# Kernel tuning notes

Measured on AMD Instinct MI355X. Metric: run time of the kernel, lower is better.

The kernel has to match this reference:

```python
import jax, jax.numpy as jnp
import numpy as np

V, E, H, L = 50257, 512, 512, 2
PAD_ID = 50256


def setup_inputs() -> dict:
    key = jax.random.key(0)
    ks = jax.random.split(key, 24)
    B, TD, TE = 16, 64, 256
    s = 0.02
    emb = jax.random.normal(ks[0], (V, E), jnp.float32) * s
    emb = emb.at[PAD_ID].set(0.0)  # padding_idx row is zero
    inp = {
        "dec_input_ids": jax.random.randint(ks[1], (B, TD), 0, V, jnp.int32),
        "initial_hidden": jax.random.normal(ks[2], (L, B, H), jnp.float32),
        "initial_cell": jax.random.normal(ks[3], (L, B, H), jnp.float32),
        "encoder_outputs": jax.random.normal(ks[4], (B, TE, H), jnp.float32),
        "src_mask": jax.random.randint(ks[5], (B, TE), 0, 2, jnp.int32),
        "emb": emb,
        "W1_w": jax.random.normal(ks[6], (H, H), jnp.float32) * s,
        "W1_b": jnp.zeros((H,), jnp.float32),
        "W2_w": jax.random.normal(ks[7], (H, H), jnp.float32) * s,
        "W2_b": jnp.zeros((H,), jnp.float32),
        "v_w": jax.random.normal(ks[8], (H,), jnp.float32) * s,
        "v_b": jnp.zeros((), jnp.float32),
        "W_ih0": jax.random.normal(ks[9], (4 * H, E + H), jnp.float32) * s,
        "W_hh0": jax.random.normal(ks[10], (4 * H, H), jnp.float32) * s,
        "b_ih0": jnp.zeros((4 * H,), jnp.float32),
        "b_hh0": jnp.zeros((4 * H,), jnp.float32),
        "W_ih1": jax.random.normal(ks[11], (4 * H, H), jnp.float32) * s,
        "W_hh1": jax.random.normal(ks[12], (4 * H, H), jnp.float32) * s,
        "b_ih1": jnp.zeros((4 * H,), jnp.float32),
        "b_hh1": jnp.zeros((4 * H,), jnp.float32),
        "fc_w": jax.random.normal(ks[13], (V, H), jnp.float32) * s,
        "fc_b": jnp.zeros((V,), jnp.float32),
    }
    return inp


def _lstm_cell(x, h, c, Wi, Wh, bi, bh):
    g = x @ Wi.T + bi + h @ Wh.T + bh  # (B, 4H)
    i, f, gg, o = jnp.split(g, 4, axis=-1)  # PyTorch gate order i,f,g,o
    i, f, o = jax.nn.sigmoid(i), jax.nn.sigmoid(f), jax.nn.sigmoid(o)
    gg = jnp.tanh(gg)
    cn = f * c + i * gg
    hn = o * jnp.tanh(cn)
    return hn, cn


def reference(dec_input_ids, initial_hidden, initial_cell, encoder_outputs, src_mask,
              emb, W1_w, W1_b, W2_w, W2_b, v_w, v_b,
              W_ih0, W_hh0, b_ih0, b_hh0, W_ih1, W_hh1, b_ih1, b_hh1,
              fc_w, fc_b):
    embedded = emb[dec_input_ids]                      # (B, T_dec, E)
    enc_proj = encoder_outputs @ W1_w.T + W1_b         # W1(encoder_outputs), (B, T_enc, H)
    pad = src_mask == 0                                # (B, T_enc)
    layers = ((W_ih0, W_hh0, b_ih0, b_hh0), (W_ih1, W_hh1, b_ih1, b_hh1))

    def step(carry, emb_t):
        h, c = carry                                   # each (L, B, H)
        q = h[-1] @ W2_w.T + W2_b                      # (B, H)
        score = jnp.tanh(enc_proj + q[:, None, :]) @ v_w + v_b  # (B, T_enc)
        score = jnp.where(pad, -1e9, score)
        attn = jax.nn.softmax(score, axis=-1)
        context = jnp.einsum('bt,bth->bh', attn, encoder_outputs)
        x = jnp.concatenate([emb_t, context], axis=-1)  # (B, E+H)
        hs, cs = [], []
        for l, (Wi, Wh, bi, bh) in enumerate(layers):
            hn, cn = _lstm_cell(x, h[l], c[l], Wi, Wh, bi, bh)
            hs.append(hn); cs.append(cn)
            x = hn
        logits_t = x @ fc_w.T + fc_b                    # (B, V)
        return (jnp.stack(hs), jnp.stack(cs)), logits_t

    _, logits = jax.lax.scan(step, (initial_hidden, initial_cell),
                             jnp.swapaxes(embedded, 0, 1))  # (T_dec, B, V)
    return jnp.swapaxes(logits, 0, 1)                       # (B, T_dec, V)
```

## Files before the change

### kernel.cpp

```cpp
#include <hip/hip_runtime.h>

#define DI __device__ __forceinline__

typedef __attribute__((ext_vector_type(2))) float f32x2;
typedef __attribute__((ext_vector_type(4))) float f32x4;
typedef __attribute__((ext_vector_type(8))) short bf16x8;
typedef __attribute__((ext_vector_type(8))) unsigned short u16x8;

constexpr int Vv = 50257, NPAD = 50304, Ee = 512, Hh = 512, Bb = 16, TDn = 64, TEn = 256;
constexpr int NBLK = 64;

constexpr size_t OFF_ENCP = 0;
constexpr size_t OFF_ENCT = OFF_ENCP + (size_t)Bb*TEn*Hh*4;
constexpr size_t OFF_G0E  = OFF_ENCT + (size_t)Bb*Hh*TEn*4;
constexpr size_t OFF_FCWB = OFF_G0E  + (size_t)TDn*Bb*4*Hh*4;
constexpr size_t OFF_H1B  = OFF_FCWB + (size_t)NPAD*Hh*2;
constexpr size_t OFF_Q    = OFF_H1B  + (size_t)TDn*Bb*Hh*2;
constexpr size_t OFF_SC   = OFF_Q    + (size_t)Bb*Hh*4;
constexpr size_t OFF_CTX  = OFF_SC   + (size_t)Bb*TEn*4;
constexpr size_t OFF_H0   = OFF_CTX  + (size_t)Bb*Hh*4;
constexpr size_t OFF_H1   = OFF_H0   + (size_t)2*Bb*Hh*4;
constexpr size_t OFF_SYNC = OFF_H1   + (size_t)2*Bb*Hh*4;

DI float dot4(f32x4 a, f32x4 b) { return a[0]*b[0] + a[1]*b[1] + a[2]*b[2] + a[3]*b[3]; }
DI float wsum(float v) { for (int m = 32; m; m >>= 1) v += __shfl_xor(v, m, 64); return v; }
DI float wmax(float v) { for (int m = 32; m; m >>= 1) v = fmaxf(v, __shfl_xor(v, m, 64)); return v; }
DI void wsum4(float& a, float& b, float& c, float& d) {
    #pragma unroll
    for (int m = 32; m; m >>= 1) {
        a += __shfl_xor(a, m, 64);
        b += __shfl_xor(b, m, 64);
        c += __shfl_xor(c, m, 64);
        d += __shfl_xor(d, m, 64);
    }
}
DI float tanhfast(float x) { float e = __expf(2.f * x); return 1.f - 2.f / (e + 1.f); }
DI float sigm(float x) { return 1.f / (1.f + __expf(-x)); }

DI int swz(int a) { return a ^ (((a >> 5) & 7) << 2); }

DI float gload1(const float* p) {
    return __hip_atomic_load(p, __ATOMIC_RELAXED, __HIP_MEMORY_SCOPE_AGENT);
}
DI void gstore1(float* p, float v) {
    __hip_atomic_store(p, v, __ATOMIC_RELAXED, __HIP_MEMORY_SCOPE_AGENT);
}
DI f32x2 gload2(const float* p) {
    unsigned long long u = __hip_atomic_load((const unsigned long long*)p,
                                             __ATOMIC_RELAXED, __HIP_MEMORY_SCOPE_AGENT);
    return __builtin_bit_cast(f32x2, u);
}
DI void gstore2(float* p, f32x2 v) {
    __hip_atomic_store((unsigned long long*)p, __builtin_bit_cast(unsigned long long, v),
                       __ATOMIC_RELAXED, __HIP_MEMORY_SCOPE_AGENT);
}
DI f32x4 gload4(const float* p) {
    f32x2 a = gload2(p), b = gload2(p + 2);
    f32x4 r; r[0] = a[0]; r[1] = a[1]; r[2] = b[0]; r[3] = b[1];
    return r;
}
DI void gstoreu16(unsigned short* p, unsigned short v) {
    __hip_atomic_store(p, v, __ATOMIC_RELAXED, __HIP_MEMORY_SCOPE_AGENT);
}

DI unsigned short f2bf(float f) {
    unsigned u = __builtin_bit_cast(unsigned, f);
    unsigned r = (u + 0x7FFFu + ((u >> 16) & 1u)) >> 16;
    return (unsigned short)r;
}
DI u16x8 cvt8(f32x4 a, f32x4 b) {
    u16x8 r;
    r[0]=f2bf(a[0]); r[1]=f2bf(a[1]); r[2]=f2bf(a[2]); r[3]=f2bf(a[3]);
    r[4]=f2bf(b[0]); r[5]=f2bf(b[1]); r[6]=f2bf(b[2]); r[7]=f2bf(b[3]);
    return r;
}

DI void gsync(unsigned* cnt, unsigned* gen, unsigned k) {
    __syncthreads();
    if (threadIdx.x == 0) {
        asm volatile("s_waitcnt vmcnt(0)" ::: "memory");
        unsigned old = __hip_atomic_fetch_add(cnt, 1u, __ATOMIC_RELAXED, __HIP_MEMORY_SCOPE_AGENT);
        if (old == k * (unsigned)NBLK - 1u) {
            __hip_atomic_store(gen, k, __ATOMIC_RELAXED, __HIP_MEMORY_SCOPE_AGENT);
        } else {
            int spins = 0;
            while (true) {
                unsigned g = __hip_atomic_load(gen, __ATOMIC_RELAXED, __HIP_MEMORY_SCOPE_AGENT);
                if (g >= k) break;
                __builtin_amdgcn_s_sleep(1);
                if ((++spins & 1023) == 0) {
                    g = __hip_atomic_load(gen, __ATOMIC_ACQUIRE, __HIP_MEMORY_SCOPE_AGENT);
                    if (g >= k) break;
                }
            }
        }
        asm volatile("" ::: "memory");
    }
    __syncthreads();
}

__global__ void prep_fcw_kernel(const float* __restrict__ src, unsigned short* __restrict__ dst) {
    size_t i = ((size_t)blockIdx.x * 256 + threadIdx.x) << 3;
    int n = (int)(i >> 9);
    u16x8 v = {0,0,0,0,0,0,0,0};
    if (n < Vv) {
        const float* p = src + i;
        v = cvt8(*(const f32x4*)p, *(const f32x4*)(p + 4));
    }
    *(u16x8*)(dst + i) = v;
}

__global__ void transpose_kernel(const float* __restrict__ enc, float* __restrict__ encT) {
    __shared__ float tile[32][33];
    const int b = blockIdx.z, e0 = blockIdx.x << 5, h0 = blockIdx.y << 5;
    const int tx = threadIdx.x, ty = threadIdx.y;
    #pragma unroll
    for (int i = 0; i < 4; ++i)
        tile[ty + i*8][tx] = enc[((size_t)(b*TEn + e0 + ty + i*8))*Hh + h0 + tx];
    __syncthreads();
    #pragma unroll
    for (int i = 0; i < 4; ++i)
        encT[((size_t)(b*Hh + h0 + ty + i*8))*TEn + e0 + tx] = tile[tx][ty + i*8];
}

template<int SRCBF, int GATHER, int OUTM>
__global__ __launch_bounds__(256, 2) void gemm_bt(
    const void* __restrict__ Av, const void* __restrict__ Bv,
    const float* __restrict__ bias, const float* __restrict__ bias2,
    float* __restrict__ Cout, int M, int N, int K, int ldb,
    const int* __restrict__ ids, int NV)
{
    __shared__ unsigned short As[128*32], Bs[128*32];
    const int tid = threadIdx.x;
    const int bn = blockIdx.x, bm = blockIdx.y;
    const int w = tid >> 6, l = tid & 63;
    const int wm = w >> 1, wn = w & 1;
    const int lr = l & 15, ls = l >> 4;
    f32x4 acc[4][4] = {};

    const int r0 = tid >> 2, c0 = (tid & 3) << 3;

    for (int kb = 0; kb < K; kb += 32) {
        #pragma unroll
        for (int half = 0; half < 2; ++half) {
            const int rr = r0 + half*64;
            {
                const int gm = bm*128 + rr;
                size_t arow = GATHER ? (size_t)ids[((gm & 15) << 6) + (gm >> 4)] : (size_t)gm;
                u16x8 v;
                if (SRCBF) {
                    v = *(const u16x8*)((const unsigned short*)Av + arow*(size_t)K + kb + c0);
                } else {
                    const float* ap = (const float*)Av + arow*(size_t)K + kb + c0;
                    v = cvt8(*(const f32x4*)ap, *(const f32x4*)(ap + 4));
                }
                *(u16x8*)&As[rr*32 + c0] = v;
            }
            {
                const size_t brow = (size_t)(bn*128 + rr);
                u16x8 v;
                if (SRCBF) {
                    v = *(const u16x8*)((const unsigned short*)Bv + brow*(size_t)ldb + kb + c0);
                } else {
                    const float* bp = (const float*)Bv + brow*(size_t)ldb + kb + c0;
                    v = cvt8(*(const f32x4*)bp, *(const f32x4*)(bp + 4));
                }
                *(u16x8*)&Bs[rr*32 + c0] = v;
            }
        }
        __syncthreads();
        bf16x8 af[4], bfv[4];
        #pragma unroll
        for (int mt = 0; mt < 4; ++mt) af[mt]  = *(const bf16x8*)&As[(wm*64 + mt*16 + lr)*32 + ls*8];
        #pragma unroll
        for (int nt = 0; nt < 4; ++nt) bfv[nt] = *(const bf16x8*)&Bs[(wn*64 + nt*16 + lr)*32 + ls*8];
        #pragma unroll
        for (int mt = 0; mt < 4; ++mt)
            #pragma unroll
            for (int nt = 0; nt < 4; ++nt)
                acc[mt][nt] = __builtin_amdgcn_mfma_f32_16x16x32_bf16(af[mt], bfv[nt], acc[mt][nt], 0, 0, 0);
        __syncthreads();
    }

    #pragma unroll
    for (int mt = 0; mt < 4; ++mt) {
        #pragma unroll
        for (int nt = 0; nt < 4; ++nt) {
            const int n = bn*128 + wn*64 + nt*16 + lr;
            const int mbase = bm*128 + wm*64 + mt*16 + ls*4;
            f32x4 a = acc[mt][nt];
            #pragma unroll
            for (int r = 0; r < 4; ++r) {
                const int m = mbase + r;
                if (OUTM == 0) {
                    float v = a[r] + bias[n] + (bias2 ? bias2[n] : 0.f);
                    Cout[(size_t)m*N + n] = v;
                } else {
                    if (n < NV) {
                        float v = a[r] + bias[n];
                        Cout[(size_t)(((m & 15) << 6) + (m >> 4))*NV + n] = v;
                    }
                }
            }
        }
    }
}

__global__ __launch_bounds__(512, 1) void recur_kernel(
    const float* __restrict__ ih, const float* __restrict__ ic,
    const float* __restrict__ W2w, const float* __restrict__ W2b,
    const float* __restrict__ vw, const float* __restrict__ vb,
    const int* __restrict__ smask,
    const float* __restrict__ Wi0, const float* __restrict__ Wh0,
    const float* __restrict__ Wi1, const float* __restrict__ Wh1,
    const float* __restrict__ bi1, const float* __restrict__ bh1,
    char* __restrict__ ws)
{
    float* encP = (float*)(ws + OFF_ENCP);
    float* encT = (float*)(ws + OFF_ENCT);
    float* g0e  = (float*)(ws + OFF_G0E);
    unsigned short* h1bf = (unsigned short*)(ws + OFF_H1B);
    float* qb  = (float*)(ws + OFF_Q);
    float* sc  = (float*)(ws + OFF_SC);
    float* ctx = (float*)(ws + OFF_CTX);
    float* h0b = (float*)(ws + OFF_H0);
    float* h1v = (float*)(ws + OFF_H1);
    unsigned* cnt = (unsigned*)(ws + OFF_SYNC);
    unsigned* gen = cnt + 64;

    __shared__ float lds[2 * Bb * Hh];

    const int tid = threadIdx.x, bid = blockIdx.x;
    const int wid = tid >> 6, l = tid & 63;
    const int j  = (bid << 3) + wid;
    const int k0 = l << 3;

    f32x4 wi0a[4], wi0b[4], wh0a[4], wh0b[4];
    f32x4 wi1a[4], wi1b[4], wh1a[4], wh1b[4];
    float bb1[4];
    #pragma unroll
    for (int g = 0; g < 4; ++g) {
        const float* p0 = Wi0 + (size_t)(g*Hh + j)*(Ee + Hh) + Ee + k0;
        wi0a[g] = *(const f32x4*)p0; wi0b[g] = *(const f32x4*)(p0 + 4);
        const float* p1 = Wh0 + (size_t)(g*Hh + j)*Hh + k0;
        wh0a[g] = *(const f32x4*)p1; wh0b[g] = *(const f32x4*)(p1 + 4);
        const float* p2 = Wi1 + (size_t)(g*Hh + j)*Hh + k0;
        wi1a[g] = *(const f32x4*)p2; wi1b[g] = *(const f32x4*)(p2 + 4);
        const float* p3 = Wh1 + (size_t)(g*Hh + j)*Hh + k0;
        wh1a[g] = *(const f32x4*)p3; wh1b[g] = *(const f32x4*)(p3 + 4);
        bb1[g] = bi1[g*Hh + j] + bh1[g*Hh + j];
    }
    const float* wr = W2w + (size_t)j*Hh + k0;
    const f32x4 w2a = *(const f32x4*)wr, w2d = *(const f32x4*)(wr + 4);
    const float w2bias = W2b[j];
    const f32x4 va = *(const f32x4*)&vw[k0], vd = *(const f32x4*)&vw[k0 + 4];
    const float vbias = vb[0];

    float c0r = (l < 16) ? ic[l*Hh + j]           : 0.f;
    float c1r = (l < 16) ? ic[Bb*Hh + l*Hh + j]   : 0.f;

    const int sb  = ((bid >> 5) << 3) | (bid & 7);
    const int u   = ((bid >> 3) & 3) * 8 + wid;
    const int se0 = u << 3;
    const int ch0 = u << 4;
    const int msk = (l < 8) ? smask[sb*TEn + se0 + l] : 1;

    for (int i = bid*512 + tid; i < (Bb*Hh) / 2; i += NBLK*512) {
        gstore2(&h0b[i*2], *(const f32x2*)&ih[i*2]);
        gstore2(&h1v[i*2], *(const f32x2*)&ih[Bb*Hh + i*2]);
    }
    unsigned bk = 0;
    gsync(cnt, gen, ++bk);

    for (int t = 0; t < TDn; ++t) {
        const int p = t & 1;
        const float* h1r = h1v + p*(Bb*Hh);
        float*       h1w = h1v + (p^1)*(Bb*Hh);
        const float* h0r = h0b + p*(Bb*Hh);
        float*       h0w = h0b + (p^1)*(Bb*Hh);

        float ge0 = 0.f, ge1 = 0.f, ge2 = 0.f, ge3 = 0.f;
        if (l < 16) {
            const float* gp = g0e + ((size_t)(t*Bb + l))*(4*Hh) + j;
            ge0 = gp[0]; ge1 = gp[Hh]; ge2 = gp[2*Hh]; ge3 = gp[3*Hh];
        }

        {
            for (int i = tid*2; i < Bb*Hh; i += 1024)
                *(f32x2*)&lds[swz(i)] = gload2(&h1r[i]);
            __syncthreads();
            float qv = 0.f;
            #pragma unroll 4
            for (int b = 0; b < Bb; ++b) {
                f32x4 ha = *(const f32x4*)&lds[swz(b*Hh + k0)];
                f32x4 hd = *(const f32x4*)&lds[swz(b*Hh + k0 + 4)];
                float s = dot4(ha, w2a) + dot4(hd, w2d);
                s = wsum(s);
                qv = (l == b) ? s + w2bias : qv;
            }
            if (l < 16) gstore1(&qb[l*Hh + j], qv);
        }
        gsync(cnt, gen, ++bk);

        {
            f32x4 qa = gload4(&qb[sb*Hh + k0]);
            f32x4 qd = gload4(&qb[sb*Hh + k0 + 4]);
            float myS = 0.f;
            #pragma unroll
            for (int i = 0; i < 8; ++i) {
                const int e = se0 + i;
                const float* ep = encP + ((size_t)(sb*TEn + e))*Hh + k0;
                f32x4 ea = *(const f32x4*)ep, ed = *(const f32x4*)(ep + 4);
                float s = 0.f;
                #pragma unroll
                for (int c = 0; c < 4; ++c)
                    s += tanhfast(ea[c] + qa[c]) * va[c] + tanhfast(ed[c] + qd[c]) * vd[c];
                s = wsum(s);
                myS = (l == i) ? s : myS;
            }
            if (l < 8)
                gstore1(&sc[sb*TEn + se0 + l], (msk == 0) ? -1e9f : (myS + vbias));
        }
        gsync(cnt, gen, ++bk);

        {
            f32x4 s4 = gload4(&sc[sb*TEn + (l << 2)]);
            float mx = wmax(fmaxf(fmaxf(s4[0], s4[1]), fmaxf(s4[2], s4[3])));
            f32x4 e4; float sm = 0.f;
            #pragma unroll
            for (int c = 0; c < 4; ++c) { e4[c] = __expf(s4[c] - mx); sm += e4[c]; }
            sm = wsum(sm);
            const float inv = 1.0f / sm;
            float myC = 0.f;
            #pragma unroll 4
            for (int i = 0; i < 16; ++i) {
                const int h = ch0 + i;
                f32x4 en = *(const f32x4*)&encT[((size_t)(sb*Hh + h))*TEn + (l << 2)];
                float s = wsum(dot4(e4, en));
                myC = (l == i) ? s : myC;
            }
            if (l < 16) gstore1(&ctx[sb*Hh + ch0 + l], myC * inv);
        }
        gsync(cnt, gen, ++bk);

        {
            for (int i = tid*2; i < Bb*Hh; i += 1024) {
                *(f32x2*)&lds[swz(i)]          = gload2(&ctx[i]);
                *(f32x2*)&lds[swz(Bb*Hh + i)]  = gload2(&h0r[i]);
            }
            __syncthreads();
            float ls0 = 0.f, ls1 = 0.f, ls2 = 0.f, ls3 = 0.f;
            #pragma unroll 4
            for (int b = 0; b < Bb; ++b) {
                f32x4 xa = *(const f32x4*)&lds[swz(b*Hh + k0)];
                f32x4 xd = *(const f32x4*)&lds[swz(b*Hh + k0 + 4)];
                f32x4 ha = *(const f32x4*)&lds[swz(Bb*Hh + b*Hh + k0)];
                f32x4 hd = *(const f32x4*)&lds[swz(Bb*Hh + b*Hh + k0 + 4)];
                float s0 = dot4(wi0a[0],xa)+dot4(wi0b[0],xd)+dot4(wh0a[0],ha)+dot4(wh0b[0],hd);
                float s1 = dot4(wi0a[1],xa)+dot4(wi0b[1],xd)+dot4(wh0a[1],ha)+dot4(wh0b[1],hd);
                float s2 = dot4(wi0a[2],xa)+dot4(wi0b[2],xd)+dot4(wh0a[2],ha)+dot4(wh0b[2],hd);
                float s3 = dot4(wi0a[3],xa)+dot4(wi0b[3],xd)+dot4(wh0a[3],ha)+dot4(wh0b[3],hd);
                wsum4(s0, s1, s2, s3);
                if (l == b) { ls0 = s0; ls1 = s1; ls2 = s2; ls3 = s3; }
            }
            if (l < 16) {
                float ii = sigm(ls0 + ge0), ff = sigm(ls1 + ge1);
                float gg = tanhfast(ls2 + ge2), oo = sigm(ls3 + ge3);
                float cn = ff*c0r + ii*gg;
                c0r = cn;
                gstore1(&h0w[l*Hh + j], oo * tanhfast(cn));
            }
        }
        gsync(cnt, gen, ++bk);

        {
            for (int i = tid*2; i < Bb*Hh; i += 1024) {
                *(f32x2*)&lds[swz(i)]          = gload2(&h0w[i]);
                *(f32x2*)&lds[swz(Bb*Hh + i)]  = gload2(&h1r[i]);
            }
            __syncthreads();
            float ls0 = 0.f, ls1 = 0.f, ls2 = 0.f, ls3 = 0.f;
            #pragma unroll 4
            for (int b = 0; b < Bb; ++b) {
                f32x4 xa = *(const f32x4*)&lds[swz(b*Hh + k0)];
                f32x4 xd = *(const f32x4*)&lds[swz(b*Hh + k0 + 4)];
                f32x4 ha = *(const f32x4*)&lds[swz(Bb*Hh + b*Hh + k0)];
                f32x4 hd = *(const f32x4*)&lds[swz(Bb*Hh + b*Hh + k0 + 4)];
                float s0 = dot4(wi1a[0],xa)+dot4(wi1b[0],xd)+dot4(wh1a[0],ha)+dot4(wh1b[0],hd);
                float s1 = dot4(wi1a[1],xa)+dot4(wi1b[1],xd)+dot4(wh1a[1],ha)+dot4(wh1b[1],hd);
                float s2 = dot4(wi1a[2],xa)+dot4(wi1b[2],xd)+dot4(wh1a[2],ha)+dot4(wh1b[2],hd);
                float s3 = dot4(wi1a[3],xa)+dot4(wi1b[3],xd)+dot4(wh1a[3],ha)+dot4(wh1b[3],hd);
                wsum4(s0, s1, s2, s3);
                if (l == b) { ls0 = s0; ls1 = s1; ls2 = s2; ls3 = s3; }
            }
            if (l < 16) {
                float ii = sigm(ls0 + bb1[0]), ff = sigm(ls1 + bb1[1]);
                float gg = tanhfast(ls2 + bb1[2]), oo = sigm(ls3 + bb1[3]);
                float cn = ff*c1r + ii*gg;
                c1r = cn;
                float hn = oo * tanhfast(cn);
                gstore1(&h1w[l*Hh + j], hn);
                gstoreu16(&h1bf[((size_t)(t*Bb + l))*Hh + j], f2bf(hn));
            }
        }
        gsync(cnt, gen, ++bk);
    }
}

extern "C" void kernel_launch(void* const* d_in, const int* in_sizes, int n_in,
                              void* d_out, int out_size, void* d_ws, size_t ws_size,
                              hipStream_t stream)
{
    const int*   ids  = (const int*)d_in[0];
    const float* ih   = (const float*)d_in[1];
    const float* ic   = (const float*)d_in[2];
    const float* enc  = (const float*)d_in[3];
    const int*   smask= (const int*)d_in[4];
    const float* emb  = (const float*)d_in[5];
    const float* W1w  = (const float*)d_in[6];
    const float* W1b  = (const float*)d_in[7];
    const float* W2w  = (const float*)d_in[8];
    const float* W2b  = (const float*)d_in[9];
    const float* vw   = (const float*)d_in[10];
    const float* vb   = (const float*)d_in[11];
    const float* Wi0  = (const float*)d_in[12];
    const float* Wh0  = (const float*)d_in[13];
    const float* bi0  = (const float*)d_in[14];
    const float* bh0  = (const float*)d_in[15];
    const float* Wi1  = (const float*)d_in[16];
    const float* Wh1  = (const float*)d_in[17];
    const float* bi1  = (const float*)d_in[18];
    const float* bh1  = (const float*)d_in[19];
    const float* fcw  = (const float*)d_in[20];
    const float* fcb  = (const float*)d_in[21];
    float* out = (float*)d_out;
    char*  ws  = (char*)d_ws;

    hipMemsetAsync(ws + OFF_SYNC, 0, 2048, stream);

    prep_fcw_kernel<<<dim3((unsigned)((size_t)NPAD*Hh/8/256)), dim3(256), 0, stream>>>(
        fcw, (unsigned short*)(ws + OFF_FCWB));

    transpose_kernel<<<dim3(TEn/32, Hh/32, Bb), dim3(32, 8), 0, stream>>>(
        enc, (float*)(ws + OFF_ENCT));

    gemm_bt<0,0,0><<<dim3(Hh/128, (Bb*TEn)/128), dim3(256), 0, stream>>>(
        enc, W1w, W1b, nullptr, (float*)(ws + OFF_ENCP),
        Bb*TEn, Hh, Hh, Hh, nullptr, 0);

    gemm_bt<0,1,0><<<dim3((4*Hh)/128, (TDn*Bb)/128), dim3(256), 0, stream>>>(
        emb, Wi0, bi0, bh0, (float*)(ws + OFF_G0E),
        TDn*Bb, 4*Hh, Ee, Ee + Hh, ids, 0);

    {
        void* args[] = { (void*)&ih, (void*)&ic, (void*)&W2w, (void*)&W2b,
                         (void*)&vw, (void*)&vb, (void*)&smask,
                         (void*)&Wi0, (void*)&Wh0, (void*)&Wi1, (void*)&Wh1,
                         (void*)&bi1, (void*)&bh1, (void*)&ws };
        hipLaunchCooperativeKernel((void*)recur_kernel, dim3(NBLK), dim3(512), args, 0, stream);
    }

    gemm_bt<1,0,1><<<dim3(NPAD/128, (TDn*Bb)/128), dim3(256), 0, stream>>>(
        ws + OFF_H1B, ws + OFF_FCWB, fcb, nullptr, out,
        TDn*Bb, NPAD, Hh, Hh, nullptr, Vv);
}
```

Before: 3.748 ms.

## Replace atomic-counter grid barrier with flag-array barrier and per-batch group barrier

Swaps the fetch-add counter grid barrier for a barrier where each block writes its own byte flag and one wavefront polls eight 64-bit words for the expected pattern. The score-to-softmax step now uses a barrier among only the 4 blocks that share a batch row, instead of a full grid barrier. Work is remapped so each group of 4 blocks handles one batch element. Global-to-LDS staging loads are widened to 4 floats. The aim is to cut barrier latency and contention on a single atomic in a latency-bound recurrent loop. It relies on byte-sized generation counters wrapping correctly and on using two alternating flag buffers.

```diff
diff --git a/kernel.cpp b/kernel.cpp
--- a/kernel.cpp
+++ b/kernel.cpp
@@ -75,26 +75,40 @@
     return r;
 }
 
-DI void gsync(unsigned* cnt, unsigned* gen, unsigned k) {
+DI void gbar(char* sy, int bid, unsigned kg) {
+    __syncthreads();
+    if (threadIdx.x < 64) {
+        unsigned long long* gf = (unsigned long long*)(sy + ((kg & 1) ? 0 : 512));
+        if (threadIdx.x == 0) {
+            asm volatile("s_waitcnt vmcnt(0)" ::: "memory");
+            char* p = (char*)(gf + (size_t)(bid >> 3) * 8) + (bid & 7);
+            __hip_atomic_store(p, (char)(unsigned char)kg, __ATOMIC_RELAXED, __HIP_MEMORY_SCOPE_AGENT);
+        }
+        const unsigned long long pat = 0x0101010101010101ULL * (unsigned char)kg;
+        const int lane = threadIdx.x;
+        for (;;) {
+            bool ok = true;
+            if (lane < 8)
+                ok = (__hip_atomic_load(gf + (size_t)lane * 8, __ATOMIC_RELAXED,
+                                        __HIP_MEMORY_SCOPE_AGENT) == pat);
+            if (__all(ok)) break;
+            __builtin_amdgcn_s_sleep(1);
+        }
+    }
+    __syncthreads();
+}
+
+DI void rbar(char* sy, int g, int u4, unsigned kr) {
     __syncthreads();
     if (threadIdx.x == 0) {
+        unsigned* gr = (unsigned*)(sy + ((kr & 1) ? 1024 : 2048));
         asm volatile("s_waitcnt vmcnt(0)" ::: "memory");
-        unsigned old = __hip_atomic_fetch_add(cnt, 1u, __ATOMIC_RELAXED, __HIP_MEMORY_SCOPE_AGENT);
-        if (old == k * (unsigned)NBLK - 1u) {
-            __hip_atomic_store(gen, k, __ATOMIC_RELAXED, __HIP_MEMORY_SCOPE_AGENT);
-        } else {
-            int spins = 0;
-            while (true) {
-                unsigned g = __hip_atomic_load(gen, __ATOMIC_RELAXED, __HIP_MEMORY_SCOPE_AGENT);
-                if (g >= k) break;
-                __builtin_amdgcn_s_sleep(1);
-                if ((++spins & 1023) == 0) {
-                    g = __hip_atomic_load(gen, __ATOMIC_ACQUIRE, __HIP_MEMORY_SCOPE_AGENT);
-                    if (g >= k) break;
-                }
-            }
-        }
-        asm volatile("" ::: "memory");
+        char* p = (char*)(gr + (size_t)g * 16) + u4;
+        __hip_atomic_store(p, (char)(unsigned char)kr, __ATOMIC_RELAXED, __HIP_MEMORY_SCOPE_AGENT);
+        const unsigned pat = 0x01010101u * (unsigned char)kr;
+        while (__hip_atomic_load(gr + (size_t)g * 16, __ATOMIC_RELAXED,
+                                 __HIP_MEMORY_SCOPE_AGENT) != pat)
+            __builtin_amdgcn_s_sleep(1);
     }
     __syncthreads();
 }
@@ -225,8 +239,7 @@
     float* ctx = (float*)(ws + OFF_CTX);
     float* h0b = (float*)(ws + OFF_H0);
     float* h1v = (float*)(ws + OFF_H1);
-    unsigned* cnt = (unsigned*)(ws + OFF_SYNC);
-    unsigned* gen = cnt + 64;
+    char* sy   = (char*)(ws + OFF_SYNC);
 
     __shared__ float lds[2 * Bb * Hh];
 
@@ -259,18 +272,19 @@
     float c0r = (l < 16) ? ic[l*Hh + j]           : 0.f;
     float c1r = (l < 16) ? ic[Bb*Hh + l*Hh + j]   : 0.f;
 
-    const int sb  = ((bid >> 5) << 3) | (bid & 7);
-    const int u   = ((bid >> 3) & 3) * 8 + wid;
-    const int se0 = u << 3;
-    const int ch0 = u << 4;
-    const int msk = (l < 8) ? smask[sb*TEn + se0 + l] : 1;
-
-    for (int i = bid*512 + tid; i < (Bb*Hh) / 2; i += NBLK*512) {
-        gstore2(&h0b[i*2], *(const f32x2*)&ih[i*2]);
-        gstore2(&h1v[i*2], *(const f32x2*)&ih[Bb*Hh + i*2]);
-    }
-    unsigned bk = 0;
-    gsync(cnt, gen, ++bk);
+    const int gb  = bid >> 2, u4 = bid & 3;
+    const int se0 = u4*64 + wid*8;
+    const int ch0 = u4*128 + wid*16;
+    const int msk = (l < 8) ? smask[gb*TEn + se0 + l] : 1;
+
+    for (int i = (bid*512 + tid)*4; i < Bb*Hh; i += NBLK*512*4) {
+        gstore2(&h0b[i],     *(const f32x2*)&ih[i]);
+        gstore2(&h0b[i + 2], *(const f32x2*)&ih[i + 2]);
+        gstore2(&h1v[i],     *(const f32x2*)&ih[Bb*Hh + i]);
+        gstore2(&h1v[i + 2], *(const f32x2*)&ih[Bb*Hh + i + 2]);
+    }
+    unsigned kg = 1, kr = 0;
+    gbar(sy, bid, kg);
 
     for (int t = 0; t < TDn; ++t) {
         const int p = t & 1;
@@ -286,8 +300,8 @@
         }
 
         {
-            for (int i = tid*2; i < Bb*Hh; i += 1024)
-                *(f32x2*)&lds[swz(i)] = gload2(&h1r[i]);
+            for (int i = tid*4; i < Bb*Hh; i += 2048)
+                *(f32x4*)&lds[swz(i)] = gload4(&h1r[i]);
             __syncthreads();
             float qv = 0.f;
             #pragma unroll 4
@@ -300,16 +314,18 @@
             }
             if (l < 16) gstore1(&qb[l*Hh + j], qv);
         }
-        gsync(cnt, gen, ++bk);
+        gbar(sy, bid, ++kg);
 
         {
-            f32x4 qa = gload4(&qb[sb*Hh + k0]);
-            f32x4 qd = gload4(&qb[sb*Hh + k0 + 4]);
+            if (tid < 128) *(f32x4*)&lds[tid*4] = gload4(&qb[gb*Hh + tid*4]);
+            __syncthreads();
+            f32x4 qa = *(const f32x4*)&lds[k0];
+            f32x4 qd = *(const f32x4*)&lds[k0 + 4];
             float myS = 0.f;
             #pragma unroll
             for (int i = 0; i < 8; ++i) {
                 const int e = se0 + i;
-                const float* ep = encP + ((size_t)(sb*TEn + e))*Hh + k0;
+                const float* ep = encP + ((size_t)(gb*TEn + e))*Hh + k0;
                 f32x4 ea = *(const f32x4*)ep, ed = *(const f32x4*)(ep + 4);
                 float s = 0.f;
                 #pragma unroll
@@ -319,12 +335,12 @@
                 myS = (l == i) ? s : myS;
             }
             if (l < 8)
-                gstore1(&sc[sb*TEn + se0 + l], (msk == 0) ? -1e9f : (myS + vbias));
-        }
-        gsync(cnt, gen, ++bk);
+                gstore1(&sc[gb*TEn + se0 + l], (msk == 0) ? -1e9f : (myS + vbias));
+        }
+        rbar(sy, gb, u4, ++kr);
 
         {
-            f32x4 s4 = gload4(&sc[sb*TEn + (l << 2)]);
+            f32x4 s4 = gload4(&sc[gb*TEn + (l << 2)]);
             float mx = wmax(fmaxf(fmaxf(s4[0], s4[1]), fmaxf(s4[2], s4[3])));
             f32x4 e4; float sm = 0.f;
             #pragma unroll
@@ -335,18 +351,18 @@
             #pragma unroll 4
             for (int i = 0; i < 16; ++i) {
                 const int h = ch0 + i;
-                f32x4 en = *(const f32x4*)&encT[((size_t)(sb*Hh + h))*TEn + (l << 2)];
+                f32x4 en = *(const f32x4*)&encT[((size_t)(gb*Hh + h))*TEn + (l << 2)];
                 float s = wsum(dot4(e4, en));
                 myC = (l == i) ? s : myC;
             }
-            if (l < 16) gstore1(&ctx[sb*Hh + ch0 + l], myC * inv);
-        }
-        gsync(cnt, gen, ++bk);
+            if (l < 16) gstore1(&ctx[gb*Hh + ch0 + l], myC * inv);
+        }
+        gbar(sy, bid, ++kg);
 
         {
-            for (int i = tid*2; i < Bb*Hh; i += 1024) {
-                *(f32x2*)&lds[swz(i)]          = gload2(&ctx[i]);
-                *(f32x2*)&lds[swz(Bb*Hh + i)]  = gload2(&h0r[i]);
+            for (int i = tid*4; i < Bb*Hh; i += 2048) {
+                *(f32x4*)&lds[swz(i)]          = gload4(&ctx[i]);
+                *(f32x4*)&lds[swz(Bb*Hh + i)]  = gload4(&h0r[i]);
             }
             __syncthreads();
             float ls0 = 0.f, ls1 = 0.f, ls2 = 0.f, ls3 = 0.f;
@@ -371,12 +387,12 @@
                 gstore1(&h0w[l*Hh + j], oo * tanhfast(cn));
             }
         }
-        gsync(cnt, gen, ++bk);
+        gbar(sy, bid, ++kg);
 
         {
-            for (int i = tid*2; i < Bb*Hh; i += 1024) {
-                *(f32x2*)&lds[swz(i)]          = gload2(&h0w[i]);
-                *(f32x2*)&lds[swz(Bb*Hh + i)]  = gload2(&h1r[i]);
+            for (int i = tid*4; i < Bb*Hh; i += 2048) {
+                *(f32x4*)&lds[swz(i)]          = gload4(&h0w[i]);
+                *(f32x4*)&lds[swz(Bb*Hh + i)]  = gload4(&h1r[i]);
             }
             __syncthreads();
             float ls0 = 0.f, ls1 = 0.f, ls2 = 0.f, ls3 = 0.f;
@@ -403,7 +419,7 @@
                 gstoreu16(&h1bf[((size_t)(t*Bb + l))*Hh + j], f2bf(hn));
             }
         }
-        gsync(cnt, gen, ++bk);
+        gbar(sy, bid, ++kg);
     }
 }
 
@@ -436,7 +452,7 @@
     float* out = (float*)d_out;
     char*  ws  = (char*)d_ws;
 
-    hipMemsetAsync(ws + OFF_SYNC, 0, 2048, stream);
+    hipMemsetAsync(ws + OFF_SYNC, 0, 4096, stream);
 
     prep_fcw_kernel<<<dim3((unsigned)((size_t)NPAD*Hh/8/256)), dim3(256), 0, stream>>>(
         fcw, (unsigned short*)(ws + OFF_FCWB));
```

Measured after the change: 3.363 ms. -10.3%, faster.
